# Performance work log

Measured on AMD Instinct MI355X. Metric: run time of the kernel, lower is better.

The kernel has to match this reference:

```python
import jax, jax.numpy as jnp
import numpy as np

NUM_BINS = 8
TAIL_BOUND = 10.0
MIN_BIN_WIDTH = 1e-3
MIN_BIN_HEIGHT = 1e-3
MIN_DERIVATIVE = 1e-3
N, D = 1048576, 32


def _knots(unnorm, min_size, bound):
    # unnorm: (D, K) -> bin sizes and cumulative knot positions in [-bound, bound]
    K = unnorm.shape[-1]
    sizes = jax.nn.softmax(unnorm, axis=-1)
    sizes = min_size + (1.0 - min_size * K) * sizes
    cum = jnp.concatenate([jnp.zeros((unnorm.shape[0], 1), unnorm.dtype), jnp.cumsum(sizes, axis=-1)], axis=-1)
    cum = 2.0 * bound * cum - bound
    cum = cum.at[:, 0].set(-bound).at[:, -1].set(bound)
    sizes = jnp.diff(cum, axis=-1)
    return sizes, cum


def _bank_log_prob(x, uw, uh, ud):
    # x: (N, D); uw, uh: (D, K); ud: (D, K-1)
    K = uw.shape[-1]
    B = TAIL_BOUND
    # linear tails: pad boundary derivatives so softplus(c)+min_deriv == 1
    c = float(np.log(np.expm1(1.0 - MIN_DERIVATIVE)))
    ud_pad = jnp.pad(ud, ((0, 0), (1, 1)), constant_values=c)            # (D, K+1)
    widths, cumw = _knots(uw, MIN_BIN_WIDTH, B)                           # (D,K),(D,K+1)
    heights, cumh = _knots(uh, MIN_BIN_HEIGHT, B)
    derivs = MIN_DERIVATIVE + jax.nn.softplus(ud_pad)                     # (D, K+1)

    inside = (x >= -B) & (x <= B)
    xc = jnp.clip(x, -B, B)
    # searchsorted per (n, d): bin index in [0, K-1]
    idx = jnp.clip(jnp.sum(xc[..., None] >= cumw[None, :, :], axis=-1) - 1, 0, K - 1)  # (N, D)

    def gather(t, i):
        return jnp.take_along_axis(t[None], i[..., None], axis=-1)[..., 0]

    cw = gather(cumw, idx)
    w = gather(widths, idx)
    ch = gather(cumh, idx)
    h = gather(heights, idx)
    d0 = gather(derivs, idx)
    d1 = gather(derivs, idx + 1)

    delta = h / w
    theta = (xc - cw) / w
    t1m = theta * (1.0 - theta)
    denom = delta + (d0 + d1 - 2.0 * delta) * t1m
    z_in = ch + h * (delta * theta * theta + d0 * t1m) / denom
    logdet_in = jnp.log(delta * delta * (d1 * theta * theta + 2.0 * delta * t1m + d0 * (1.0 - theta) ** 2)) - 2.0 * jnp.log(denom)

    z = jnp.where(inside, z_in, x)            # identity outside [-B, B]
    logdet = jnp.where(inside, logdet_in, 0.0)
    log2pi = float(np.log(2.0 * np.pi))
    return -0.5 * z * z - 0.5 * log2pi + logdet  # (N, D) per-dim log-prob


def setup_inputs() -> dict:
    key = jax.random.key(0)
    kx, kw, kh, kd = jax.random.split(key, 4)
    return {
        "x": 3.0 * jax.random.normal(kx, (N, D), dtype=jnp.float32),
        "unnorm_widths": jax.random.normal(kw, (D, NUM_BINS), dtype=jnp.float32),
        "unnorm_heights": jax.random.normal(kh, (D, NUM_BINS), dtype=jnp.float32),
        "unnorm_derivs": jax.random.normal(kd, (D, NUM_BINS - 1), dtype=jnp.float32),
    }


def reference(x, unnorm_widths, unnorm_heights, unnorm_derivs):
    return _bank_log_prob(x, unnorm_widths, unnorm_heights, unnorm_derivs)
```

## Files before the change

kernel.cpp:

```cpp
#include <hip/hip_runtime.h>
#include <math.h>

#define NB 8
#define DD 32
constexpr float TB   = 10.0f;
constexpr float MBW  = 1e-3f;
constexpr float MBH  = 1e-3f;
constexpr float MDER = 1e-3f;

__device__ __forceinline__ float softplusf(float v) {
    return (v > 20.0f) ? v : log1pf(expf(v));
}

__global__ __launch_bounds__(256) void mfb_kernel(
    const float* __restrict__ x,
    const float* __restrict__ uw,
    const float* __restrict__ uh,
    const float* __restrict__ ud,
    float* __restrict__ out,
    int n4)
{
    __shared__ float  s_kn[DD][NB + 1];
    __shared__ float4 s_A[DD][NB];
    __shared__ float4 s_B[DD][NB];

    const int t = threadIdx.x;

    if (t < DD) {
        float posw[NB + 1], posh[NB + 1];
        {
            float u[NB];
            float m = -1e30f;
            #pragma unroll
            for (int k = 0; k < NB; ++k) { u[k] = uw[t * NB + k]; m = fmaxf(m, u[k]); }
            float s = 0.0f;
            #pragma unroll
            for (int k = 0; k < NB; ++k) { u[k] = expf(u[k] - m); s += u[k]; }
            const float inv = 1.0f / s;
            posw[0] = -TB;
            float cum = 0.0f;
            #pragma unroll
            for (int k = 0; k < NB; ++k) {
                cum += MBW + (1.0f - MBW * (float)NB) * (u[k] * inv);
                posw[k + 1] = 2.0f * TB * cum - TB;
            }
            posw[NB] = TB;
        }
        {
            float u[NB];
            float m = -1e30f;
            #pragma unroll
            for (int k = 0; k < NB; ++k) { u[k] = uh[t * NB + k]; m = fmaxf(m, u[k]); }
            float s = 0.0f;
            #pragma unroll
            for (int k = 0; k < NB; ++k) { u[k] = expf(u[k] - m); s += u[k]; }
            const float inv = 1.0f / s;
            posh[0] = -TB;
            float cum = 0.0f;
            #pragma unroll
            for (int k = 0; k < NB; ++k) {
                cum += MBH + (1.0f - MBH * (float)NB) * (u[k] * inv);
                posh[k + 1] = 2.0f * TB * cum - TB;
            }
            posh[NB] = TB;
        }
        float dv[NB + 1];
        {
            const float c   = logf(expm1f(1.0f - MDER));
            const float bnd = MDER + softplusf(c);
            dv[0]  = bnd;
            dv[NB] = bnd;
            #pragma unroll
            for (int k = 1; k < NB; ++k)
                dv[k] = MDER + softplusf(ud[t * (NB - 1) + (k - 1)]);
        }
        #pragma unroll
        for (int k = 0; k <= NB; ++k) s_kn[t][k] = posw[k];
        const int key = (t >> 2) & 7;
        #pragma unroll
        for (int b = 0; b < NB; ++b) {
            const float w     = posw[b + 1] - posw[b];
            const float h     = posh[b + 1] - posh[b];
            const float invw  = 1.0f / w;
            const float delta = h * invw;
            const float s2    = dv[b] + dv[b + 1] - 2.0f * delta;
            s_A[t][b ^ key] = make_float4(posw[b], invw, posh[b], h);
            s_B[t][b ^ key] = make_float4(dv[b], dv[b + 1], delta, s2);
        }
    }
    __syncthreads();

    constexpr float HALF_LOG_2PI = 0.91893853320467274178f;

    const int i0     = blockIdx.x * blockDim.x + t;
    const int stride = gridDim.x * blockDim.x;
    const int dbase  = (i0 * 4) & (DD - 1);
    const int key    = (dbase >> 2) & 7;

    float kn[4][7];
    #pragma unroll
    for (int j = 0; j < 4; ++j)
        #pragma unroll
        for (int k = 0; k < 7; ++k)
            kn[j][k] = s_kn[dbase + j][k + 1];

    auto evalone = [&](float xx, int j) -> float {
        const float xc = fminf(fmaxf(xx, -TB), TB);
        int idx = 0;
        #pragma unroll
        for (int k = 0; k < 7; ++k) idx += (xc >= kn[j][k]) ? 1 : 0;

        const int bb = idx ^ key;
        const float4 A = s_A[dbase + j][bb];
        const float4 B = s_B[dbase + j][bb];

        const float theta = (xc - A.x) * A.y;
        const float tt    = theta * theta;
        const float omt   = 1.0f - theta;
        const float t1m   = theta * omt;
        const float denom = fmaf(B.w, t1m, B.z);
        const float rden  = __builtin_amdgcn_rcpf(denom);
        const float zin   = fmaf(A.w * fmaf(B.z, tt, B.x * t1m), rden, A.z);
        const float twod  = B.z + B.z;
        const float p     = fmaf(B.y, tt, fmaf(twod, t1m, B.x * (omt * omt)));
        const float num   = (B.z * B.z) * p;
        const float ld    = __logf(num * rden * rden);

        const bool inside = fabsf(xx) <= TB;
        const float z   = inside ? zin : xx;
        const float acc = inside ? ld : 0.0f;
        return fmaf(z * z, -0.5f, acc) - HALF_LOG_2PI;
    };

    const float4* __restrict__ x4 = reinterpret_cast<const float4*>(x);
    float4* __restrict__ o4 = reinterpret_cast<float4*>(out);

    for (int i = i0; i < n4; i += stride) {
        const float4 xv = x4[i];
        float4 r;
        r.x = evalone(xv.x, 0);
        r.y = evalone(xv.y, 1);
        r.z = evalone(xv.z, 2);
        r.w = evalone(xv.w, 3);
        o4[i] = r;
    }
}

extern "C" void kernel_launch(void* const* d_in, const int* in_sizes, int n_in,
                              void* d_out, int out_size, void* d_ws, size_t ws_size,
                              hipStream_t stream) {
    const float* x  = (const float*)d_in[0];
    const float* uw = (const float*)d_in[1];
    const float* uh = (const float*)d_in[2];
    const float* ud = (const float*)d_in[3];
    float* out = (float*)d_out;

    const int n4 = in_sizes[0] / 4;
    int blocks = (n4 + 255) / 256;
    if (blocks > 2048) blocks = 2048;

    mfb_kernel<<<blocks, 256, 0, stream>>>(x, uw, uh, ud, out, n4);
}
```

Before: 61.40 us.

## Pack spline bin table into one fp16-compressed float4 and use float2 accesses

Replaces the two per-bin float4 shared tables with a single float4 that stores knot position and inverse width in fp32, and cumulative height, height and both derivatives as packed fp16. Delta and the slope term are recomputed in registers, which halves the shared-memory lookups per element. Each thread now handles two columns with float2 loads, processes two strided float2 chunks per iteration, and keeps its knot thresholds in registers pinned with an empty asm. The fp16 storage of heights and derivatives lowers precision and may break tolerance, and the log-determinant is no longer masked to zero outside the bound.

New measurement: 74.91 us. +22.0%, slower.

```diff
diff --git a/kernel.cpp b/kernel.cpp
--- a/kernel.cpp
+++ b/kernel.cpp
@@ -1,4 +1,5 @@
 #include <hip/hip_runtime.h>
+#include <hip/hip_fp16.h>
 #include <math.h>
 
 #define NB 8
@@ -18,16 +19,15 @@
     const float* __restrict__ uh,
     const float* __restrict__ ud,
     float* __restrict__ out,
-    int n4)
+    int total2)
 {
-    __shared__ float  s_kn[DD][NB + 1];
-    __shared__ float4 s_A[DD][NB];
-    __shared__ float4 s_B[DD][NB];
+    __shared__ float4 s_T[DD][NB + 1];
+    __shared__ float  s_kn[DD][7];
 
     const int t = threadIdx.x;
 
     if (t < DD) {
-        float posw[NB + 1], posh[NB + 1];
+        float posw[NB + 1], posh[NB + 1], dv[NB + 1];
         {
             float u[NB];
             float m = -1e30f;
@@ -64,7 +64,6 @@
             }
             posh[NB] = TB;
         }
-        float dv[NB + 1];
         {
             const float c   = logf(expm1f(1.0f - MDER));
             const float bnd = MDER + softplusf(c);
@@ -75,74 +74,103 @@
                 dv[k] = MDER + softplusf(ud[t * (NB - 1) + (k - 1)]);
         }
         #pragma unroll
-        for (int k = 0; k <= NB; ++k) s_kn[t][k] = posw[k];
-        const int key = (t >> 2) & 7;
+        for (int k = 0; k < 7; ++k) s_kn[t][k] = posw[k + 1];
         #pragma unroll
         for (int b = 0; b < NB; ++b) {
-            const float w     = posw[b + 1] - posw[b];
-            const float h     = posh[b + 1] - posh[b];
-            const float invw  = 1.0f / w;
-            const float delta = h * invw;
-            const float s2    = dv[b] + dv[b + 1] - 2.0f * delta;
-            s_A[t][b ^ key] = make_float4(posw[b], invw, posh[b], h);
-            s_B[t][b ^ key] = make_float4(dv[b], dv[b + 1], delta, s2);
+            const float w    = posw[b + 1] - posw[b];
+            const float h    = posh[b + 1] - posh[b];
+            const float invw = 1.0f / w;
+            const unsigned u1 = ((unsigned)__half_as_ushort(__float2half_rn(h)) << 16)
+                              |  (unsigned)__half_as_ushort(__float2half_rn(posh[b]));
+            const unsigned u2 = ((unsigned)__half_as_ushort(__float2half_rn(dv[b + 1])) << 16)
+                              |  (unsigned)__half_as_ushort(__float2half_rn(dv[b]));
+            float4 T;
+            T.x = posw[b];
+            T.y = invw;
+            T.z = __uint_as_float(u1);
+            T.w = __uint_as_float(u2);
+            s_T[t][b] = T;
         }
     }
     __syncthreads();
 
     constexpr float HALF_LOG_2PI = 0.91893853320467274178f;
 
-    const int i0     = blockIdx.x * blockDim.x + t;
+    const int g      = blockIdx.x * blockDim.x + t;
     const int stride = gridDim.x * blockDim.x;
-    const int dbase  = (i0 * 4) & (DD - 1);
-    const int key    = (dbase >> 2) & 7;
+    const int dbase  = (g * 2) & (DD - 1);
 
-    float kn[4][7];
-    #pragma unroll
-    for (int j = 0; j < 4; ++j)
-        #pragma unroll
-        for (int k = 0; k < 7; ++k)
-            kn[j][k] = s_kn[dbase + j][k + 1];
+    float a0 = s_kn[dbase][0], a1 = s_kn[dbase][1], a2 = s_kn[dbase][2],
+          a3 = s_kn[dbase][3], a4 = s_kn[dbase][4], a5 = s_kn[dbase][5],
+          a6 = s_kn[dbase][6];
+    float b0 = s_kn[dbase + 1][0], b1 = s_kn[dbase + 1][1], b2 = s_kn[dbase + 1][2],
+          b3 = s_kn[dbase + 1][3], b4 = s_kn[dbase + 1][4], b5 = s_kn[dbase + 1][5],
+          b6 = s_kn[dbase + 1][6];
+    const float4* __restrict__ rowA = s_T[dbase];
+    const float4* __restrict__ rowB = s_T[dbase + 1];
 
-    auto evalone = [&](float xx, int j) -> float {
+    auto evalone = [&](float xx,
+                       float k0, float k1, float k2, float k3, float k4, float k5, float k6,
+                       const float4* __restrict__ row) -> float {
         const float xc = fminf(fmaxf(xx, -TB), TB);
         int idx = 0;
-        #pragma unroll
-        for (int k = 0; k < 7; ++k) idx += (xc >= kn[j][k]) ? 1 : 0;
+        idx += (xc >= k0) ? 1 : 0;
+        idx += (xc >= k1) ? 1 : 0;
+        idx += (xc >= k2) ? 1 : 0;
+        idx += (xc >= k3) ? 1 : 0;
+        idx += (xc >= k4) ? 1 : 0;
+        idx += (xc >= k5) ? 1 : 0;
+        idx += (xc >= k6) ? 1 : 0;
 
-        const int bb = idx ^ key;
-        const float4 A = s_A[dbase + j][bb];
-        const float4 B = s_B[dbase + j][bb];
+        const float4 T = row[idx];
+        const unsigned u1 = __float_as_uint(T.z);
+        const unsigned u2 = __float_as_uint(T.w);
+        const float ch = __half2float(__ushort_as_half((unsigned short)(u1 & 0xffffu)));
+        const float h  = __half2float(__ushort_as_half((unsigned short)(u1 >> 16)));
+        const float d0 = __half2float(__ushort_as_half((unsigned short)(u2 & 0xffffu)));
+        const float d1 = __half2float(__ushort_as_half((unsigned short)(u2 >> 16)));
 
-        const float theta = (xc - A.x) * A.y;
+        const float delta = h * T.y;
+        const float twod  = delta + delta;
+        const float s2    = (d0 + d1) - twod;
+        const float theta = (xc - T.x) * T.y;
         const float tt    = theta * theta;
         const float omt   = 1.0f - theta;
         const float t1m   = theta * omt;
-        const float denom = fmaf(B.w, t1m, B.z);
+        const float denom = fmaf(s2, t1m, delta);
         const float rden  = __builtin_amdgcn_rcpf(denom);
-        const float zin   = fmaf(A.w * fmaf(B.z, tt, B.x * t1m), rden, A.z);
-        const float twod  = B.z + B.z;
-        const float p     = fmaf(B.y, tt, fmaf(twod, t1m, B.x * (omt * omt)));
-        const float num   = (B.z * B.z) * p;
-        const float ld    = __logf(num * rden * rden);
-
-        const bool inside = fabsf(xx) <= TB;
-        const float z   = inside ? zin : xx;
-        const float acc = inside ? ld : 0.0f;
-        return fmaf(z * z, -0.5f, acc) - HALF_LOG_2PI;
+        const float zin   = fmaf(h * fmaf(delta, tt, d0 * t1m), rden, ch);
+        const float p     = fmaf(d1, tt, fmaf(twod, t1m, d0 * (omt * omt)));
+        const float ld    = __logf(((delta * delta) * p) * (rden * rden));
+        const float z = (fabsf(xx) <= TB) ? zin : xx;
+        return fmaf(z * z, -0.5f, ld) - HALF_LOG_2PI;
     };
 
-    const float4* __restrict__ x4 = reinterpret_cast<const float4*>(x);
-    float4* __restrict__ o4 = reinterpret_cast<float4*>(out);
+    const float2* __restrict__ x2 = reinterpret_cast<const float2*>(x);
+    float2* __restrict__ o2 = reinterpret_cast<float2*>(out);
 
-    for (int i = i0; i < n4; i += stride) {
-        const float4 xv = x4[i];
-        float4 r;
-        r.x = evalone(xv.x, 0);
-        r.y = evalone(xv.y, 1);
-        r.z = evalone(xv.z, 2);
-        r.w = evalone(xv.w, 3);
-        o4[i] = r;
+    int i = g;
+    for (; i + stride < total2; i += 2 * stride) {
+        asm volatile("" : "+v"(a0), "+v"(a1), "+v"(a2), "+v"(a3), "+v"(a4),
+                          "+v"(a5), "+v"(a6),
+                          "+v"(b0), "+v"(b1), "+v"(b2), "+v"(b3), "+v"(b4),
+                          "+v"(b5), "+v"(b6));
+        const float2 va = x2[i];
+        const float2 vb = x2[i + stride];
+        float2 ra, rb;
+        ra.x = evalone(va.x, a0, a1, a2, a3, a4, a5, a6, rowA);
+        ra.y = evalone(va.y, b0, b1, b2, b3, b4, b5, b6, rowB);
+        rb.x = evalone(vb.x, a0, a1, a2, a3, a4, a5, a6, rowA);
+        rb.y = evalone(vb.y, b0, b1, b2, b3, b4, b5, b6, rowB);
+        o2[i] = ra;
+        o2[i + stride] = rb;
+    }
+    for (; i < total2; i += stride) {
+        const float2 va = x2[i];
+        float2 ra;
+        ra.x = evalone(va.x, a0, a1, a2, a3, a4, a5, a6, rowA);
+        ra.y = evalone(va.y, b0, b1, b2, b3, b4, b5, b6, rowB);
+        o2[i] = ra;
     }
 }
 
@@ -155,9 +183,9 @@
     const float* ud = (const float*)d_in[3];
     float* out = (float*)d_out;
 
-    const int n4 = in_sizes[0] / 4;
-    int blocks = (n4 + 255) / 256;
+    const int total2 = in_sizes[0] / 2;
+    int blocks = (total2 + 255) / 256;
     if (blocks > 2048) blocks = 2048;
 
-    mfb_kernel<<<blocks, 256, 0, stream>>>(x, uw, uh, ud, out, n4);
+    mfb_kernel<<<blocks, 256, 0, stream>>>(x, uw, uh, ud, out, total2);
 }
```

## Precompute spline coefficients into one packed table and process two float4 per iteration

Applied to the files above, without the earlier changes.

Packs per-bin coefficients into a single interleaved float4 table of premultiplied terms. Evaluation becomes a few FMAs plus one rcp and one log2, and the explicit inside/outside select for the log-det is dropped, since the boundary derivatives make that term vanish at the clamped edges. The grid-stride loop is unrolled to load two float4 vectors per iteration for more memory-level parallelism. It also adds an occupancy hint to launch_bounds. Because the kernel is close to HBM bandwidth-bound, fewer ALU ops may help only a little, and the log-det term outside the bounds is now only approximately zero.

Measured after the change: 60.33 us. About the same (-1.7%).

```diff
diff --git a/kernel.cpp b/kernel.cpp
--- a/kernel.cpp
+++ b/kernel.cpp
@@ -12,7 +12,7 @@
     return (v > 20.0f) ? v : log1pf(expf(v));
 }
 
-__global__ __launch_bounds__(256) void mfb_kernel(
+__global__ __launch_bounds__(256, 4) void mfb_kernel(
     const float* __restrict__ x,
     const float* __restrict__ uw,
     const float* __restrict__ uh,
@@ -20,14 +20,13 @@
     float* __restrict__ out,
     int n4)
 {
-    __shared__ float  s_kn[DD][NB + 1];
-    __shared__ float4 s_A[DD][NB];
-    __shared__ float4 s_B[DD][NB];
+    __shared__ float4 s_T[DD][2 * NB + 1];
+    __shared__ float  s_kn[DD][7];
 
     const int t = threadIdx.x;
 
     if (t < DD) {
-        float posw[NB + 1], posh[NB + 1];
+        float posw[NB + 1], posh[NB + 1], dv[NB + 1];
         {
             float u[NB];
             float m = -1e30f;
@@ -64,7 +63,6 @@
             }
             posh[NB] = TB;
         }
-        float dv[NB + 1];
         {
             const float c   = logf(expm1f(1.0f - MDER));
             const float bnd = MDER + softplusf(c);
@@ -75,7 +73,7 @@
                 dv[k] = MDER + softplusf(ud[t * (NB - 1) + (k - 1)]);
         }
         #pragma unroll
-        for (int k = 0; k <= NB; ++k) s_kn[t][k] = posw[k];
+        for (int k = 0; k < 7; ++k) s_kn[t][k] = posw[k + 1];
         const int key = (t >> 2) & 7;
         #pragma unroll
         for (int b = 0; b < NB; ++b) {
@@ -83,66 +81,103 @@
             const float h     = posh[b + 1] - posh[b];
             const float invw  = 1.0f / w;
             const float delta = h * invw;
-            const float s2    = dv[b] + dv[b + 1] - 2.0f * delta;
-            s_A[t][b ^ key] = make_float4(posw[b], invw, posh[b], h);
-            s_B[t][b ^ key] = make_float4(dv[b], dv[b + 1], delta, s2);
+            const float d0    = dv[b];
+            const float d1    = dv[b + 1];
+            const float s2    = (d0 + d1) - 2.0f * delta;
+            const int   bb    = b ^ key;
+            s_T[t][2 * bb]     = make_float4(invw, -posw[b] * invw,
+                                             h * (delta - d0), h * d0);
+            s_T[t][2 * bb + 1] = make_float4(posh[b], delta, s2, d0);
         }
     }
     __syncthreads();
 
     constexpr float HALF_LOG_2PI = 0.91893853320467274178f;
+    constexpr float LN2          = 0.69314718055994530942f;
 
-    const int i0     = blockIdx.x * blockDim.x + t;
+    const int g      = blockIdx.x * blockDim.x + t;
     const int stride = gridDim.x * blockDim.x;
-    const int dbase  = (i0 * 4) & (DD - 1);
+    const int dbase  = (g * 4) & (DD - 1);
     const int key    = (dbase >> 2) & 7;
 
-    float kn[4][7];
-    #pragma unroll
-    for (int j = 0; j < 4; ++j)
-        #pragma unroll
-        for (int k = 0; k < 7; ++k)
-            kn[j][k] = s_kn[dbase + j][k + 1];
+    float a0 = s_kn[dbase + 0][0], a1 = s_kn[dbase + 0][1], a2 = s_kn[dbase + 0][2],
+          a3 = s_kn[dbase + 0][3], a4 = s_kn[dbase + 0][4], a5 = s_kn[dbase + 0][5],
+          a6 = s_kn[dbase + 0][6];
+    float b0 = s_kn[dbase + 1][0], b1 = s_kn[dbase + 1][1], b2 = s_kn[dbase + 1][2],
+          b3 = s_kn[dbase + 1][3], b4 = s_kn[dbase + 1][4], b5 = s_kn[dbase + 1][5],
+          b6 = s_kn[dbase + 1][6];
+    float c0 = s_kn[dbase + 2][0], c1 = s_kn[dbase + 2][1], c2 = s_kn[dbase + 2][2],
+          c3 = s_kn[dbase + 2][3], c4 = s_kn[dbase + 2][4], c5 = s_kn[dbase + 2][5],
+          c6 = s_kn[dbase + 2][6];
+    float e0 = s_kn[dbase + 3][0], e1 = s_kn[dbase + 3][1], e2 = s_kn[dbase + 3][2],
+          e3 = s_kn[dbase + 3][3], e4 = s_kn[dbase + 3][4], e5 = s_kn[dbase + 3][5],
+          e6 = s_kn[dbase + 3][6];
 
-    auto evalone = [&](float xx, int j) -> float {
-        const float xc = fminf(fmaxf(xx, -TB), TB);
+    const float4* __restrict__ r0 = &s_T[dbase + 0][0];
+    const float4* __restrict__ r1 = &s_T[dbase + 1][0];
+    const float4* __restrict__ r2 = &s_T[dbase + 2][0];
+    const float4* __restrict__ r3 = &s_T[dbase + 3][0];
+
+    auto evalone = [&](float xx,
+                       float k0, float k1, float k2, float k3, float k4, float k5, float k6,
+                       const float4* __restrict__ row) -> float {
         int idx = 0;
-        #pragma unroll
-        for (int k = 0; k < 7; ++k) idx += (xc >= kn[j][k]) ? 1 : 0;
+        idx += (xx >= k0) ? 1 : 0;
+        idx += (xx >= k1) ? 1 : 0;
+        idx += (xx >= k2) ? 1 : 0;
+        idx += (xx >= k3) ? 1 : 0;
+        idx += (xx >= k4) ? 1 : 0;
+        idx += (xx >= k5) ? 1 : 0;
+        idx += (xx >= k6) ? 1 : 0;
 
-        const int bb = idx ^ key;
-        const float4 A = s_A[dbase + j][bb];
-        const float4 B = s_B[dbase + j][bb];
+        const float4* p = row + 2 * (idx ^ key);
+        const float4 W0 = p[0];
+        const float4 W1 = p[1];
 
-        const float theta = (xc - A.x) * A.y;
-        const float tt    = theta * theta;
-        const float omt   = 1.0f - theta;
-        const float t1m   = theta * omt;
-        const float denom = fmaf(B.w, t1m, B.z);
-        const float rden  = __builtin_amdgcn_rcpf(denom);
-        const float zin   = fmaf(A.w * fmaf(B.z, tt, B.x * t1m), rden, A.z);
-        const float twod  = B.z + B.z;
-        const float p     = fmaf(B.y, tt, fmaf(twod, t1m, B.x * (omt * omt)));
-        const float num   = (B.z * B.z) * p;
-        const float ld    = __logf(num * rden * rden);
-
-        const bool inside = fabsf(xx) <= TB;
-        const float z   = inside ? zin : xx;
-        const float acc = inside ? ld : 0.0f;
-        return fmaf(z * z, -0.5f, acc) - HALF_LOG_2PI;
+        const float xc    = fminf(fmaxf(xx, -TB), TB);
+        const float theta = fmaf(xc, W0.x, W0.y);
+        const float u     = fmaf(-theta, theta, theta);
+        const float den   = fmaf(W1.z, u, W1.y);
+        const float rden  = __builtin_amdgcn_rcpf(den);
+        const float num1  = theta * fmaf(theta, W0.z, W0.w);
+        const float zin   = fmaf(num1, rden, W1.x);
+        const float dmd   = W1.y - W1.w;
+        const float poly  = fmaf(fmaf(W1.z, theta, dmd + dmd), theta, W1.w);
+        const float ee    = W1.y * rden;
+        const float larg  = poly * (ee * ee);
+        const float lg2   = __log2f(larg);
+        const float z  = (fabsf(xx) <= TB) ? zin : xx;
+        const float ld = fmaf(lg2, LN2, -HALF_LOG_2PI);
+        return fmaf(z * z, -0.5f, ld);
     };
 
     const float4* __restrict__ x4 = reinterpret_cast<const float4*>(x);
     float4* __restrict__ o4 = reinterpret_cast<float4*>(out);
 
-    for (int i = i0; i < n4; i += stride) {
-        const float4 xv = x4[i];
-        float4 r;
-        r.x = evalone(xv.x, 0);
-        r.y = evalone(xv.y, 1);
-        r.z = evalone(xv.z, 2);
-        r.w = evalone(xv.w, 3);
-        o4[i] = r;
+    int i = g;
+    for (; i + stride < n4; i += 2 * stride) {
+        const float4 xa = x4[i];
+        const float4 xb = x4[i + stride];
+        float4 ra, rb;
+        ra.x = evalone(xa.x, a0, a1, a2, a3, a4, a5, a6, r0);
+        ra.y = evalone(xa.y, b0, b1, b2, b3, b4, b5, b6, r1);
+        ra.z = evalone(xa.z, c0, c1, c2, c3, c4, c5, c6, r2);
+        ra.w = evalone(xa.w, e0, e1, e2, e3, e4, e5, e6, r3);
+        rb.x = evalone(xb.x, a0, a1, a2, a3, a4, a5, a6, r0);
+        rb.y = evalone(xb.y, b0, b1, b2, b3, b4, b5, b6, r1);
+        rb.z = evalone(xb.z, c0, c1, c2, c3, c4, c5, c6, r2);
+        rb.w = evalone(xb.w, e0, e1, e2, e3, e4, e5, e6, r3);
+        o4[i] = ra;
+        o4[i + stride] = rb;
+    }
+    for (; i < n4; i += stride) {
+        const float4 xa = x4[i];
+        float4 ra;
+        ra.x = evalone(xa.x, a0, a1, a2, a3, a4, a5, a6, r0);
+        ra.y = evalone(xa.y, b0, b1, b2, b3, b4, b5, b6, r1);
+        ra.z = evalone(xa.z, c0, c1, c2, c3, c4, c5, c6, r2);
+        ra.w = evalone(xa.w, e0, e1, e2, e3, e4, e5, e6, r3);
+        o4[i] = ra;
     }
 }
 
```
